# Optimization experiments

Measured on AMD Instinct MI355X. Metric: run time of the kernel, lower is better.

Reference implementation:

```python
import jax, jax.numpy as jnp
import numpy as np

GROUPS = 32
EPS = 1e-5


def group_norm(x, w, b):
    B, C, H, W = x.shape
    xg = x.reshape(B, GROUPS, C // GROUPS, H, W)
    mu = xg.mean(axis=(2, 3, 4), keepdims=True)
    var = xg.var(axis=(2, 3, 4), keepdims=True)
    xg = (xg - mu) * jax.lax.rsqrt(var + EPS)
    return xg.reshape(B, C, H, W) * w[None, :, None, None] + b[None, :, None, None]


def conv1x1(x, w, b):
    # 1x1 conv == per-position GEMM over channels
    return jnp.einsum('bchw,dc->bdhw', x, w) + b[None, :, None, None]


def setup_inputs() -> dict:
    key = jax.random.key(0)
    ks = jax.random.split(key, 8)
    B, C, H, W = 16, 512, 32, 32
    scale = C ** -0.5  # keep pre-softmax logits well-conditioned
    return {
        'x': jax.random.normal(ks[0], (B, C, H, W), jnp.float32),
        'temb': jax.random.normal(ks[1], (B, C), jnp.float32),
        'gn_w': jnp.ones((C,), jnp.float32),
        'gn_b': jnp.zeros((C,), jnp.float32),
        'q_w': jax.random.normal(ks[2], (C, C), jnp.float32) * scale,
        'q_b': jnp.zeros((C,), jnp.float32),
        'k_w': jax.random.normal(ks[3], (C, C), jnp.float32) * scale,
        'k_b': jnp.zeros((C,), jnp.float32),
        'v_w': jax.random.normal(ks[4], (C, C), jnp.float32) * scale,
        'v_b': jnp.zeros((C,), jnp.float32),
        'p_w': jax.random.normal(ks[5], (C, C), jnp.float32) * scale,
        'p_b': jnp.zeros((C,), jnp.float32),
    }


def reference(x, temb, gn_w, gn_b, q_w, q_b, k_w, k_b, v_w, v_b, p_w, p_b):
    B, C, H, W = x.shape
    h = group_norm(x, gn_w, gn_b)
    q = conv1x1(h, q_w, q_b)
    k = conv1x1(h, k_w, k_b)
    v = conv1x1(h, v_w, v_b)
    # spatial self-attention: every (h,w) query attends over all (H,W) keys
    scores = jnp.einsum('bchw,bcHW->bhwHW', q, k) * (C ** -0.5)  # [B,H,W,H,W]
    attn = jax.nn.softmax(scores.reshape(B, H, W, H * W), axis=-1).reshape(B, H, W, H, W)
    h = jnp.einsum('bhwHW,bcHW->bchw', attn, v)
    return x + conv1x1(h, p_w, p_b)
```

## Files before the change

### kernel.cpp

```cpp
#include <hip/hip_runtime.h>

typedef unsigned short u16;
typedef __bf16 bf16x8 __attribute__((ext_vector_type(8)));
typedef float f32x4 __attribute__((ext_vector_type(4)));
typedef unsigned short u16x8 __attribute__((ext_vector_type(8)));

__device__ __forceinline__ u16 f2bf(float f) {
  unsigned u = __builtin_bit_cast(unsigned, f);
  u += 0x7fffu + ((u >> 16) & 1u);
  return (u16)(u >> 16);
}
__device__ __forceinline__ float b2f(u16 h) {
  return __builtin_bit_cast(float, (unsigned)h << 16);
}

__device__ __forceinline__ void gld16(const u16* g, u16* l) {
  __builtin_amdgcn_global_load_lds((const __attribute__((address_space(1))) unsigned int*)g,
                                   (__attribute__((address_space(3))) unsigned int*)l, 16, 0, 0);
}

__global__ __launch_bounds__(256) void cvt_kernel(const float* __restrict__ qw, const float* __restrict__ kw,
                                                  const float* __restrict__ vw, const float* __restrict__ pw,
                                                  const float* __restrict__ qb, const float* __restrict__ kb,
                                                  u16* __restrict__ wqk, u16* __restrict__ wv,
                                                  u16* __restrict__ wp, float* __restrict__ qkb,
                                                  float scale) {
  if (blockIdx.y == 4) {
    int i = blockIdx.x * 256 + threadIdx.x;
    if (i < 512) qkb[i] = qb[i] * scale;
    else if (i < 1024) qkb[i] = kb[i - 512];
    return;
  }
  const float* s;
  u16* o;
  float sc = 1.f;
  switch (blockIdx.y) {
    case 0: s = qw; o = wqk; sc = scale; break;
    case 1: s = kw; o = wqk + 262144; break;
    case 2: s = vw; o = wv; break;
    default: s = pw; o = wp; break;
  }
  int i = (blockIdx.x * 256 + threadIdx.x) * 4;
  float4 v = *(const float4*)(s + i);
  ushort4 pk = { f2bf(v.x * sc), f2bf(v.y * sc), f2bf(v.z * sc), f2bf(v.w * sc) };
  *(ushort4*)&o[i] = pk;
}

#define GN_ROW 1026

__global__ __launch_bounds__(256) void gn_kernel(const float* __restrict__ x, const float* __restrict__ w,
                                                 const float* __restrict__ bias, u16* __restrict__ hn) {
  __shared__ u16 tile[16 * GN_ROW];
  __shared__ float red[18];
  const int tid = threadIdx.x;
  const int bb = blockIdx.x >> 5;
  const int g = blockIdx.x & 31;
  const float4* xb = (const float4*)(x + ((size_t)bb * 512 + (size_t)g * 16) * 1024);

  float s = 0.f, sq = 0.f;
#pragma unroll
  for (int j = 0; j < 16; ++j) {
    float4 v = xb[j * 256 + tid];
    s += v.x + v.y + v.z + v.w;
    sq += v.x * v.x + v.y * v.y + v.z * v.z + v.w * v.w;
    int base = j * GN_ROW + tid * 4;
    ushort2 p0 = { f2bf(v.x), f2bf(v.y) };
    ushort2 p1 = { f2bf(v.z), f2bf(v.w) };
    *(ushort2*)&tile[base] = p0;
    *(ushort2*)&tile[base + 2] = p1;
  }
#pragma unroll
  for (int o = 32; o; o >>= 1) {
    s += __shfl_down(s, o, 64);
    sq += __shfl_down(sq, o, 64);
  }
  const int wv = tid >> 6;
  if ((tid & 63) == 0) { red[wv] = s; red[wv + 4] = sq; }
  __syncthreads();
  if (tid == 0) {
    float S = red[0] + red[1] + red[2] + red[3];
    float Q = red[4] + red[5] + red[6] + red[7];
    float mean = S * (1.f / 16384.f);
    float var = Q * (1.f / 16384.f) - mean * mean;
    red[16] = mean;
    red[17] = rsqrtf(var + 1e-5f);
  }
  __syncthreads();
  const float mean = red[16], rstd = red[17];
  const int c0 = g * 16;

  float wf[16], bf_[16];
#pragma unroll
  for (int c = 0; c < 16; ++c) {
    float wc = w[c0 + c];
    wf[c] = wc * rstd;
    bf_[c] = bias[c0 + c] - mean * rstd * wc;
  }
#pragma unroll
  for (int it = 0; it < 4; ++it) {
    int hw = it * 256 + tid;
    u16x8 lo{}, hi{};
#pragma unroll
    for (int c = 0; c < 8; ++c) {
      lo[c] = f2bf(b2f(tile[c * GN_ROW + hw]) * wf[c] + bf_[c]);
      hi[c] = f2bf(b2f(tile[(c + 8) * GN_ROW + hw]) * wf[c + 8] + bf_[c + 8]);
    }
    u16* dst = hn + ((size_t)bb * 1024 + hw) * 512 + c0;
    *(u16x8*)dst = lo;
    *(u16x8*)(dst + 8) = hi;
  }
}

template <int BM, int BN, int MINW, typename OutT>
__global__ __launch_bounds__(BM * BN / 64, MINW) void gemm_nt(
    const u16* __restrict__ A, const u16* __restrict__ Bt, OutT* __restrict__ C,
    const float* __restrict__ bias_m, const float* __restrict__ bias_n, const float* __restrict__ res,
    int K, int lda, int ldb, int ldc, size_t sA, size_t sB, size_t sC, size_t sRes,
    int T, int lognbx) {
  constexpr int TPB = BM * BN / 64;
  constexpr int WGN = BN / 64;
  constexpr int ASLOT = 4 * BM / TPB;
  constexpr int BSLOT = 4 * BN / TPB;
  __shared__ u16 lsA[2][BM * 32];
  __shared__ u16 lsB[2][BN * 32];

  int fi = blockIdx.x;
  const int halfT = T << 3;
  const int h = (fi >= halfT);
  fi -= h * halfT;
  const int tile = fi >> 3;
  const int zb = (fi & 7) + (h << 3);
  const int bx = tile & ((1 << lognbx) - 1);
  const int by = tile >> lognbx;

  const int tid = threadIdx.x;
  const int lane = tid & 63;
  const int wave = tid >> 6;
  const int wm = wave / WGN, wn = wave % WGN;
  const int tm = by * BM, tn = bx * BN;
  const u16* Ab = A + (size_t)zb * sA;
  const u16* Bb = Bt + (size_t)zb * sB;

  f32x4 acc[4][4] = {};
  const int q = lane >> 4, r = lane & 15;

  const u16* pA[ASLOT];
  const u16* pB[BSLOT];
#pragma unroll
  for (int i = 0; i < ASLOT; ++i) {
    int e = tid + i * TPB;
    int ra = e >> 2, sl = e & 3;
    int g = sl ^ ((ra >> 1) & 3);
    pA[i] = Ab + (size_t)(tm + ra) * lda + g * 8;
  }
#pragma unroll
  for (int i = 0; i < BSLOT; ++i) {
    int e = tid + i * TPB;
    int ra = e >> 2, sl = e & 3;
    int g = sl ^ ((ra >> 1) & 3);
    pB[i] = Bb + (size_t)(tn + ra) * ldb + g * 8;
  }

#pragma unroll
  for (int i = 0; i < ASLOT; ++i) gld16(pA[i], &lsA[0][(tid + i * TPB) * 8]);
#pragma unroll
  for (int i = 0; i < BSLOT; ++i) gld16(pB[i], &lsB[0][(tid + i * TPB) * 8]);
  __syncthreads();

  int offA[4], offB[4];
#pragma unroll
  for (int mt = 0; mt < 4; ++mt) {
    int rowa = wm * 64 + mt * 16 + r;
    offA[mt] = rowa * 32 + (q ^ ((rowa >> 1) & 3)) * 8;
    int rowb = wn * 64 + mt * 16 + r;
    offB[mt] = rowb * 32 + (q ^ ((rowb >> 1) & 3)) * 8;
  }

  const int nk = K >> 5;
  for (int k = 0; k < nk; ++k) {
    const int cur = k & 1;
    if (k + 1 < nk) {
      const int k0 = (k + 1) << 5;
#pragma unroll
      for (int i = 0; i < ASLOT; ++i) gld16(pA[i] + k0, &lsA[cur ^ 1][(tid + i * TPB) * 8]);
#pragma unroll
      for (int i = 0; i < BSLOT; ++i) gld16(pB[i] + k0, &lsB[cur ^ 1][(tid + i * TPB) * 8]);
    }
    bf16x8 af[4], bfv[4];
#pragma unroll
    for (int mt = 0; mt < 4; ++mt) {
      af[mt] = *(const bf16x8*)(const void*)&lsA[cur][offA[mt]];
      bfv[mt] = *(const bf16x8*)(const void*)&lsB[cur][offB[mt]];
    }
#pragma unroll
    for (int mt = 0; mt < 4; ++mt)
#pragma unroll
      for (int nt = 0; nt < 4; ++nt)
        acc[mt][nt] = __builtin_amdgcn_mfma_f32_16x16x32_bf16(af[mt], bfv[nt], acc[mt][nt], 0, 0, 0);
    __syncthreads();
  }

  OutT* Cb = C + (size_t)zb * sC;
  const float* Rb = res ? res + (size_t)zb * sRes : nullptr;
#pragma unroll
  for (int mt = 0; mt < 4; ++mt) {
#pragma unroll
    for (int nt = 0; nt < 4; ++nt) {
      const int col = tn + wn * 64 + nt * 16 + r;
      const float bn = bias_n ? bias_n[col] : 0.f;
#pragma unroll
      for (int reg = 0; reg < 4; ++reg) {
        const int row = tm + wm * 64 + mt * 16 + q * 4 + reg;
        float v = acc[mt][nt][reg];
        const float bm = bias_m ? bias_m[row] : 0.f;
        v = v + bm + bn;
        const size_t idx = (size_t)row * ldc + col;
        if (Rb) v += Rb[idx];
        if constexpr (__is_same(OutT, u16)) Cb[idx] = f2bf(v);
        else Cb[idx] = v;
      }
    }
  }
}

__global__ __launch_bounds__(256) void softmax_kernel(u16* __restrict__ S) {
  const int row = blockIdx.x * 4 + (threadIdx.x >> 6);
  const int lane = threadIdx.x & 63;
  u16* p = S + (size_t)row * 1024;
  u16x8 a = *(const u16x8*)(p + lane * 8);
  u16x8 b = *(const u16x8*)(p + 512 + lane * 8);
  float va[8], vb[8];
  float m = -3.0e38f;
#pragma unroll
  for (int j = 0; j < 8; ++j) {
    va[j] = b2f(a[j]);
    vb[j] = b2f(b[j]);
    m = fmaxf(m, fmaxf(va[j], vb[j]));
  }
#pragma unroll
  for (int o = 32; o; o >>= 1) m = fmaxf(m, __shfl_xor(m, o, 64));
  float s = 0.f;
#pragma unroll
  for (int j = 0; j < 8; ++j) {
    va[j] = __expf(va[j] - m);
    vb[j] = __expf(vb[j] - m);
    s += va[j] + vb[j];
  }
#pragma unroll
  for (int o = 32; o; o >>= 1) s += __shfl_xor(s, o, 64);
  const float inv = 1.f / s;
  u16x8 oa, ob;
#pragma unroll
  for (int j = 0; j < 8; ++j) {
    oa[j] = f2bf(va[j] * inv);
    ob[j] = f2bf(vb[j] * inv);
  }
  *(u16x8*)(p + lane * 8) = oa;
  *(u16x8*)(p + 512 + lane * 8) = ob;
}

extern "C" void kernel_launch(void* const* d_in, const int* in_sizes, int n_in,
                              void* d_out, int out_size, void* d_ws, size_t ws_size,
                              hipStream_t stream) {
  const float* x = (const float*)d_in[0];
  const float* gn_w = (const float*)d_in[2];
  const float* gn_b = (const float*)d_in[3];
  const float* q_w = (const float*)d_in[4];
  const float* q_b = (const float*)d_in[5];
  const float* k_w = (const float*)d_in[6];
  const float* k_b = (const float*)d_in[7];
  const float* v_w = (const float*)d_in[8];
  const float* v_b = (const float*)d_in[9];
  const float* p_w = (const float*)d_in[10];
  const float* p_b = (const float*)d_in[11];
  float* out = (float*)d_out;

  u16* wqk = (u16*)d_ws;
  u16* wv = wqk + 524288;
  u16* wp = wv + 262144;
  float* qkb = (float*)(wp + 262144);
  u16* hn = wp + 262144 + 2048;
  u16* qkt = hn + 8388608;
  u16* vv = qkt + 16777216;
  u16* ot = vv + 8388608;
  u16* Sb = ot + 8388608;

  const float inv_sqrt_c = 0.044194173824159216f;
  const size_t sHN = 524288, sS = 1048576;

  cvt_kernel<<<dim3(256, 5), 256, 0, stream>>>(q_w, k_w, v_w, p_w, q_b, k_b, wqk, wv, wp, qkb, inv_sqrt_c);
  gn_kernel<<<512, 256, 0, stream>>>(x, gn_w, gn_b, hn);

  gemm_nt<256, 256, 4, u16><<<256, 1024, 0, stream>>>(hn, wqk, qkt, nullptr, qkb, nullptr,
                                                      512, 512, 512, 1024, sHN, 0, sS, 0, 16, 2);
  gemm_nt<128, 128, 3, u16><<<512, 256, 0, stream>>>(wv, hn, vv, v_b, nullptr, nullptr,
                                                     512, 512, 512, 1024, 0, sHN, sHN, 0, 32, 3);
  gemm_nt<256, 256, 4, u16><<<256, 1024, 0, stream>>>(qkt, qkt + 512, Sb, nullptr, nullptr, nullptr,
                                                      512, 1024, 1024, 1024, sS, sS, sS, 0, 16, 2);
  softmax_kernel<<<4096, 256, 0, stream>>>(Sb);
  gemm_nt<128, 128, 3, u16><<<512, 256, 0, stream>>>(Sb, vv, ot, nullptr, nullptr, nullptr,
                                                     1024, 1024, 1024, 512, sS, sHN, sHN, 0, 32, 2);
  gemm_nt<128, 128, 3, float><<<512, 256, 0, stream>>>(wp, ot, out, p_b, nullptr, x,
                                                       512, 512, 512, 1024, 0, sHN, sHN, sHN, 32, 3);
}
```

Measured before the change: 262.7 us.

## Deepen GEMM LDS pipeline to four stages with vmcnt-based waits and setprio

```diff
diff --git a/kernel.cpp b/kernel.cpp
--- a/kernel.cpp
+++ b/kernel.cpp
@@ -121,8 +121,9 @@
   constexpr int WGN = BN / 64;
   constexpr int ASLOT = 4 * BM / TPB;
   constexpr int BSLOT = 4 * BN / TPB;
-  __shared__ u16 lsA[2][BM * 32];
-  __shared__ u16 lsB[2][BN * 32];
+  constexpr int LPT = ASLOT + BSLOT;
+  __shared__ u16 lsA[4][BM * 32];
+  __shared__ u16 lsB[4][BN * 32];
 
   int fi = blockIdx.x;
   const int halfT = T << 3;
@@ -161,12 +162,6 @@
     pB[i] = Bb + (size_t)(tn + ra) * ldb + g * 8;
   }
 
-#pragma unroll
-  for (int i = 0; i < ASLOT; ++i) gld16(pA[i], &lsA[0][(tid + i * TPB) * 8]);
-#pragma unroll
-  for (int i = 0; i < BSLOT; ++i) gld16(pB[i], &lsB[0][(tid + i * TPB) * 8]);
-  __syncthreads();
-
   int offA[4], offB[4];
 #pragma unroll
   for (int mt = 0; mt < 4; ++mt) {
@@ -177,14 +172,25 @@
   }
 
   const int nk = K >> 5;
-  for (int k = 0; k < nk; ++k) {
-    const int cur = k & 1;
-    if (k + 1 < nk) {
-      const int k0 = (k + 1) << 5;
-#pragma unroll
-      for (int i = 0; i < ASLOT; ++i) gld16(pA[i] + k0, &lsA[cur ^ 1][(tid + i * TPB) * 8]);
-#pragma unroll
-      for (int i = 0; i < BSLOT; ++i) gld16(pB[i] + k0, &lsB[cur ^ 1][(tid + i * TPB) * 8]);
+
+#pragma unroll
+  for (int t = 0; t < 3; ++t) {
+    const int k0 = t << 5;
+#pragma unroll
+    for (int i = 0; i < ASLOT; ++i) gld16(pA[i] + k0, &lsA[t][(tid + i * TPB) * 8]);
+#pragma unroll
+    for (int i = 0; i < BSLOT; ++i) gld16(pB[i] + k0, &lsB[t][(tid + i * TPB) * 8]);
+  }
+
+  auto body = [&](int k) {
+    const int cur = k & 3;
+    if (k + 3 < nk) {
+      const int k0 = (k + 3) << 5;
+      const int nb = (k + 3) & 3;
+#pragma unroll
+      for (int i = 0; i < ASLOT; ++i) gld16(pA[i] + k0, &lsA[nb][(tid + i * TPB) * 8]);
+#pragma unroll
+      for (int i = 0; i < BSLOT; ++i) gld16(pB[i] + k0, &lsB[nb][(tid + i * TPB) * 8]);
     }
     bf16x8 af[4], bfv[4];
 #pragma unroll
@@ -192,13 +198,26 @@
       af[mt] = *(const bf16x8*)(const void*)&lsA[cur][offA[mt]];
       bfv[mt] = *(const bf16x8*)(const void*)&lsB[cur][offB[mt]];
     }
+    __builtin_amdgcn_s_setprio(1);
 #pragma unroll
     for (int mt = 0; mt < 4; ++mt)
 #pragma unroll
       for (int nt = 0; nt < 4; ++nt)
         acc[mt][nt] = __builtin_amdgcn_mfma_f32_16x16x32_bf16(af[mt], bfv[nt], acc[mt][nt], 0, 0, 0);
-    __syncthreads();
-  }
+    __builtin_amdgcn_s_setprio(0);
+  };
+
+  for (int k = 0; k < nk - 2; ++k) {
+    asm volatile("s_waitcnt vmcnt(%0)" ::"n"(2 * LPT) : "memory");
+    __builtin_amdgcn_s_barrier();
+    body(k);
+  }
+  asm volatile("s_waitcnt vmcnt(%0)" ::"n"(LPT) : "memory");
+  __builtin_amdgcn_s_barrier();
+  body(nk - 2);
+  asm volatile("s_waitcnt vmcnt(0)" ::: "memory");
+  __builtin_amdgcn_s_barrier();
+  body(nk - 1);
 
   OutT* Cb = C + (size_t)zb * sC;
   const float* Rb = res ? res + (size_t)zb * sRes : nullptr;
```

New measurement: 263.8 us. Within noise of the previous version (+0.4%).

## Fuse softmax into PV GEMM and retile smaller GEMMs to 64x128

Applied to the files above, without the earlier changes.

```diff
diff --git a/kernel.cpp b/kernel.cpp
--- a/kernel.cpp
+++ b/kernel.cpp
@@ -111,14 +111,17 @@
   }
 }
 
-template <int BM, int BN, int MINW, typename OutT>
-__global__ __launch_bounds__(BM * BN / 64, MINW) void gemm_nt(
+template <int BM, int BN, int TPB, int MINW, typename OutT>
+__global__ __launch_bounds__(TPB, MINW) void gemm_nt(
     const u16* __restrict__ A, const u16* __restrict__ Bt, OutT* __restrict__ C,
     const float* __restrict__ bias_m, const float* __restrict__ bias_n, const float* __restrict__ res,
     int K, int lda, int ldb, int ldc, size_t sA, size_t sB, size_t sC, size_t sRes,
     int T, int lognbx) {
-  constexpr int TPB = BM * BN / 64;
+  constexpr int NW = TPB / 64;
   constexpr int WGN = BN / 64;
+  constexpr int WGM = NW / WGN;
+  constexpr int WTM = BM / WGM;
+  constexpr int MT = WTM / 16;
   constexpr int ASLOT = 4 * BM / TPB;
   constexpr int BSLOT = 4 * BN / TPB;
   __shared__ u16 lsA[2][BM * 32];
@@ -141,7 +144,7 @@
   const u16* Ab = A + (size_t)zb * sA;
   const u16* Bb = Bt + (size_t)zb * sB;
 
-  f32x4 acc[4][4] = {};
+  f32x4 acc[MT][4] = {};
   const int q = lane >> 4, r = lane & 15;
 
   const u16* pA[ASLOT];
@@ -167,13 +170,16 @@
   for (int i = 0; i < BSLOT; ++i) gld16(pB[i], &lsB[0][(tid + i * TPB) * 8]);
   __syncthreads();
 
-  int offA[4], offB[4];
-#pragma unroll
-  for (int mt = 0; mt < 4; ++mt) {
-    int rowa = wm * 64 + mt * 16 + r;
+  int offA[MT], offB[4];
+#pragma unroll
+  for (int mt = 0; mt < MT; ++mt) {
+    int rowa = wm * WTM + mt * 16 + r;
     offA[mt] = rowa * 32 + (q ^ ((rowa >> 1) & 3)) * 8;
-    int rowb = wn * 64 + mt * 16 + r;
-    offB[mt] = rowb * 32 + (q ^ ((rowb >> 1) & 3)) * 8;
+  }
+#pragma unroll
+  for (int nt = 0; nt < 4; ++nt) {
+    int rowb = wn * 64 + nt * 16 + r;
+    offB[nt] = rowb * 32 + (q ^ ((rowb >> 1) & 3)) * 8;
   }
 
   const int nk = K >> 5;
@@ -186,14 +192,13 @@
 #pragma unroll
       for (int i = 0; i < BSLOT; ++i) gld16(pB[i] + k0, &lsB[cur ^ 1][(tid + i * TPB) * 8]);
     }
-    bf16x8 af[4], bfv[4];
-#pragma unroll
-    for (int mt = 0; mt < 4; ++mt) {
-      af[mt] = *(const bf16x8*)(const void*)&lsA[cur][offA[mt]];
-      bfv[mt] = *(const bf16x8*)(const void*)&lsB[cur][offB[mt]];
-    }
-#pragma unroll
-    for (int mt = 0; mt < 4; ++mt)
+    bf16x8 af[MT], bfv[4];
+#pragma unroll
+    for (int mt = 0; mt < MT; ++mt) af[mt] = *(const bf16x8*)(const void*)&lsA[cur][offA[mt]];
+#pragma unroll
+    for (int nt = 0; nt < 4; ++nt) bfv[nt] = *(const bf16x8*)(const void*)&lsB[cur][offB[nt]];
+#pragma unroll
+    for (int mt = 0; mt < MT; ++mt)
 #pragma unroll
       for (int nt = 0; nt < 4; ++nt)
         acc[mt][nt] = __builtin_amdgcn_mfma_f32_16x16x32_bf16(af[mt], bfv[nt], acc[mt][nt], 0, 0, 0);
@@ -203,14 +208,14 @@
   OutT* Cb = C + (size_t)zb * sC;
   const float* Rb = res ? res + (size_t)zb * sRes : nullptr;
 #pragma unroll
-  for (int mt = 0; mt < 4; ++mt) {
+  for (int mt = 0; mt < MT; ++mt) {
 #pragma unroll
     for (int nt = 0; nt < 4; ++nt) {
       const int col = tn + wn * 64 + nt * 16 + r;
       const float bn = bias_n ? bias_n[col] : 0.f;
 #pragma unroll
       for (int reg = 0; reg < 4; ++reg) {
-        const int row = tm + wm * 64 + mt * 16 + q * 4 + reg;
+        const int row = tm + wm * WTM + mt * 16 + q * 4 + reg;
         float v = acc[mt][nt][reg];
         const float bm = bias_m ? bias_m[row] : 0.f;
         v = v + bm + bn;
@@ -223,40 +228,138 @@
   }
 }
 
-__global__ __launch_bounds__(256) void softmax_kernel(u16* __restrict__ S) {
-  const int row = blockIdx.x * 4 + (threadIdx.x >> 6);
-  const int lane = threadIdx.x & 63;
-  u16* p = S + (size_t)row * 1024;
-  u16x8 a = *(const u16x8*)(p + lane * 8);
-  u16x8 b = *(const u16x8*)(p + 512 + lane * 8);
-  float va[8], vb[8];
-  float m = -3.0e38f;
-#pragma unroll
-  for (int j = 0; j < 8; ++j) {
-    va[j] = b2f(a[j]);
-    vb[j] = b2f(b[j]);
-    m = fmaxf(m, fmaxf(va[j], vb[j]));
-  }
-#pragma unroll
-  for (int o = 32; o; o >>= 1) m = fmaxf(m, __shfl_xor(m, o, 64));
-  float s = 0.f;
-#pragma unroll
-  for (int j = 0; j < 8; ++j) {
-    va[j] = __expf(va[j] - m);
-    vb[j] = __expf(vb[j] - m);
-    s += va[j] + vb[j];
-  }
-#pragma unroll
-  for (int o = 32; o; o >>= 1) s += __shfl_xor(s, o, 64);
-  const float inv = 1.f / s;
-  u16x8 oa, ob;
-#pragma unroll
-  for (int j = 0; j < 8; ++j) {
-    oa[j] = f2bf(va[j] * inv);
-    ob[j] = f2bf(vb[j] * inv);
-  }
-  *(u16x8*)(p + lane * 8) = oa;
-  *(u16x8*)(p + 512 + lane * 8) = ob;
+__global__ __launch_bounds__(256, 4) void gemm_pv(const u16* __restrict__ S, const u16* __restrict__ V,
+                                                  u16* __restrict__ O) {
+  __shared__ u16 lsA[2][64 * 32];
+  __shared__ u16 lsB[2][128 * 32];
+
+  int fi = blockIdx.x;
+  const int halfT = 64 << 3;
+  const int h = (fi >= halfT);
+  fi -= h * halfT;
+  const int tile = fi >> 3;
+  const int zb = (fi & 7) + (h << 3);
+  const int bx = tile & 3;
+  const int by = tile >> 2;
+
+  const int tid = threadIdx.x;
+  const int lane = tid & 63;
+  const int wave = tid >> 6;
+  const int wm = wave >> 1, wn = wave & 1;
+  const int tm = by * 64, tn = bx * 128;
+  const u16* Ab = S + (size_t)zb * 1048576;
+  const u16* Bb = V + (size_t)zb * 524288;
+
+  const int ra = tid >> 2, g4 = tid & 3;
+  {
+  }
+  const u16* rowp = Ab + (size_t)(tm + ra) * 1024 + g4 * 256;
+  float m = -3.0e38f, s = 0.f;
+#pragma unroll 4
+  for (int j = 0; j < 32; ++j) {
+    u16x8 cv = *(const u16x8*)(rowp + j * 8);
+    float v[8];
+    float cm = -3.0e38f;
+#pragma unroll
+    for (int t = 0; t < 8; ++t) {
+      v[t] = b2f(cv[t]);
+      cm = fmaxf(cm, v[t]);
+    }
+    if (cm > m) {
+      s *= __expf(m - cm);
+      m = cm;
+    }
+#pragma unroll
+    for (int t = 0; t < 8; ++t) s += __expf(v[t] - m);
+  }
+#pragma unroll
+  for (int o = 1; o <= 2; o <<= 1) {
+    float mo = __shfl_xor(m, o, 64);
+    float so = __shfl_xor(s, o, 64);
+    float M = fmaxf(m, mo);
+    s = s * __expf(m - M) + so * __expf(mo - M);
+    m = M;
+  }
+  const float is_ = 1.f / s;
+
+  const int waA = ra * 32 + (g4 ^ ((ra >> 1) & 3)) * 8;
+  const u16* pA = Ab + (size_t)(tm + ra) * 1024 + g4 * 8;
+  const u16* pB[2];
+#pragma unroll
+  for (int i = 0; i < 2; ++i) {
+    int e = tid + i * 256;
+    int rb = e >> 2, sl = e & 3;
+    int g = sl ^ ((rb >> 1) & 3);
+    pB[i] = Bb + (size_t)(tn + rb) * 1024 + g * 8;
+  }
+
+  {
+    u16x8 a0 = *(const u16x8*)pA;
+    u16x8 t0;
+#pragma unroll
+    for (int t = 0; t < 8; ++t) t0[t] = f2bf(__expf(b2f(a0[t]) - m) * is_);
+    *(u16x8*)&lsA[0][waA] = t0;
+  }
+#pragma unroll
+  for (int i = 0; i < 2; ++i) gld16(pB[i], &lsB[0][(tid + i * 256) * 8]);
+  __syncthreads();
+
+  const int q = lane >> 4, r = lane & 15;
+  int offA[2], offB[4];
+#pragma unroll
+  for (int mt = 0; mt < 2; ++mt) {
+    int rowa = wm * 32 + mt * 16 + r;
+    offA[mt] = rowa * 32 + (q ^ ((rowa >> 1) & 3)) * 8;
+  }
+#pragma unroll
+  for (int nt = 0; nt < 4; ++nt) {
+    int rowb = wn * 64 + nt * 16 + r;
+    offB[nt] = rowb * 32 + (q ^ ((rowb >> 1) & 3)) * 8;
+  }
+
+  f32x4 acc[2][4] = {};
+  const int nk = 32;
+  for (int k = 0; k < nk; ++k) {
+    const int cur = k & 1;
+    u16x8 an;
+    if (k + 1 < nk) {
+      const int k0 = (k + 1) << 5;
+      an = *(const u16x8*)(pA + k0);
+#pragma unroll
+      for (int i = 0; i < 2; ++i) gld16(pB[i] + k0, &lsB[cur ^ 1][(tid + i * 256) * 8]);
+    }
+    bf16x8 af[2], bfv[4];
+#pragma unroll
+    for (int mt = 0; mt < 2; ++mt) af[mt] = *(const bf16x8*)(const void*)&lsA[cur][offA[mt]];
+#pragma unroll
+    for (int nt = 0; nt < 4; ++nt) bfv[nt] = *(const bf16x8*)(const void*)&lsB[cur][offB[nt]];
+#pragma unroll
+    for (int mt = 0; mt < 2; ++mt)
+#pragma unroll
+      for (int nt = 0; nt < 4; ++nt)
+        acc[mt][nt] = __builtin_amdgcn_mfma_f32_16x16x32_bf16(af[mt], bfv[nt], acc[mt][nt], 0, 0, 0);
+    if (k + 1 < nk) {
+      u16x8 tn8;
+#pragma unroll
+      for (int t = 0; t < 8; ++t) tn8[t] = f2bf(__expf(b2f(an[t]) - m) * is_);
+      *(u16x8*)&lsA[cur ^ 1][waA] = tn8;
+    }
+    __syncthreads();
+  }
+
+  u16* Ob = O + (size_t)zb * 524288;
+#pragma unroll
+  for (int mt = 0; mt < 2; ++mt) {
+#pragma unroll
+    for (int nt = 0; nt < 4; ++nt) {
+      const int col = tn + wn * 64 + nt * 16 + r;
+#pragma unroll
+      for (int reg = 0; reg < 4; ++reg) {
+        const int row = tm + wm * 32 + mt * 16 + q * 4 + reg;
+        Ob[(size_t)row * 512 + col] = f2bf(acc[mt][nt][reg]);
+      }
+    }
+  }
 }
 
 extern "C" void kernel_launch(void* const* d_in, const int* in_sizes, int n_in,
@@ -291,15 +394,13 @@
   cvt_kernel<<<dim3(256, 5), 256, 0, stream>>>(q_w, k_w, v_w, p_w, q_b, k_b, wqk, wv, wp, qkb, inv_sqrt_c);
   gn_kernel<<<512, 256, 0, stream>>>(x, gn_w, gn_b, hn);
 
-  gemm_nt<256, 256, 4, u16><<<256, 1024, 0, stream>>>(hn, wqk, qkt, nullptr, qkb, nullptr,
-                                                      512, 512, 512, 1024, sHN, 0, sS, 0, 16, 2);
-  gemm_nt<128, 128, 3, u16><<<512, 256, 0, stream>>>(wv, hn, vv, v_b, nullptr, nullptr,
-                                                     512, 512, 512, 1024, 0, sHN, sHN, 0, 32, 3);
-  gemm_nt<256, 256, 4, u16><<<256, 1024, 0, stream>>>(qkt, qkt + 512, Sb, nullptr, nullptr, nullptr,
-                                                      512, 1024, 1024, 1024, sS, sS, sS, 0, 16, 2);
-  softmax_kernel<<<4096, 256, 0, stream>>>(Sb);
-  gemm_nt<128, 128, 3, u16><<<512, 256, 0, stream>>>(Sb, vv, ot, nullptr, nullptr, nullptr,
-                                                     1024, 1024, 1024, 512, sS, sHN, sHN, 0, 32, 2);
-  gemm_nt<128, 128, 3, float><<<512, 256, 0, stream>>>(wp, ot, out, p_b, nullptr, x,
-                                                       512, 512, 512, 1024, 0, sHN, sHN, sHN, 32, 3);
-}
+  gemm_nt<256, 256, 1024, 8, u16><<<256, 1024, 0, stream>>>(hn, wqk, qkt, nullptr, qkb, nullptr,
+                                                            512, 512, 512, 1024, sHN, 0, sS, 0, 16, 2);
+  gemm_nt<64, 128, 256, 4, u16><<<1024, 256, 0, stream>>>(wv, hn, vv, v_b, nullptr, nullptr,
+                                                          512, 512, 512, 1024, 0, sHN, sHN, 0, 64, 3);
+  gemm_nt<256, 256, 1024, 8, u16><<<256, 1024, 0, stream>>>(qkt, qkt + 512, Sb, nullptr, nullptr, nullptr,
+                                                            512, 1024, 1024, 1024, sS, sS, sS, 0, 16, 2);
+  gemm_pv<<<1024, 256, 0, stream>>>(Sb, vv, ot);
+  gemm_nt<64, 128, 256, 4, float><<<1024, 256, 0, stream>>>(wp, ot, out, p_b, nullptr, x,
+                                                            512, 512, 512, 1024, 0, sHN, sHN, sHN, 64, 3);
+}
```

Result: slower. 593.1 us (+125.8%).
